# Optimization experiments

Hardware: AMD Instinct MI355X
Metric: run time of the kernel (lower is better)

## Reference

```python
import jax, jax.numpy as jnp
import numpy as np

COMMITMENT_COST = 0.25


def setup_inputs() -> dict:
    key = jax.random.key(0)
    k1, k2 = jax.random.split(key)
    inputs = jax.random.normal(k1, (8, 1024, 512), dtype=jnp.float32)
    codebook = jax.random.normal(k2, (8192, 512), dtype=jnp.float32)
    return {"inputs": inputs, "codebook": codebook}


def reference(inputs, codebook):
    B, S, D = inputs.shape
    flat = inputs.reshape(-1, D)  # [N, D]
    distances = (
        jnp.sum(flat * flat, axis=1, keepdims=True)
        + jnp.sum(codebook * codebook, axis=1)
        - 2.0 * flat @ codebook.T
    )
    encoding_indices = jnp.argmin(distances, axis=1)  # [N] int
    min_distances = jnp.min(distances, axis=1)  # [N]
    quantized = codebook[encoding_indices].reshape(inputs.shape)  # [B,S,D]
    # straight-through estimator
    quantized_st = inputs + jax.lax.stop_gradient(quantized - inputs)
    # mse losses with reduction='sum'; .detach() -> stop_gradient
    loss_vq = jnp.sum((quantized - jax.lax.stop_gradient(inputs)) ** 2)
    loss_commit = jnp.sum((inputs - jax.lax.stop_gradient(quantized)) ** 2)
    # non-EMA branch: loss = commitment_cost * loss_commit + loss_vq
    loss = loss_commit * COMMITMENT_COST + loss_vq
    return (
        quantized_st,
        loss,
        encoding_indices.reshape(B, S),
        min_distances.reshape(B, S),
        loss_commit,
    )
```

## Files before the change

### kernel.cpp

```cpp
#include <hip/hip_runtime.h>

typedef __attribute__((ext_vector_type(8)))  short short8;
typedef __attribute__((ext_vector_type(16))) float f32x16;
typedef unsigned short ushort_t;
typedef unsigned int uint32;

#define NROWS 8192
#define NCODE 8192
#define DIM   512

#define OUT_Q      0
#define OUT_LOSS   4194304
#define OUT_IDX    4194305
#define OUT_MIND   4202497
#define OUT_COMMIT 4210689

#define WS_ENORM  0
#define WS_PMIN   8192
#define WS_PIDX   73728
#define WS_LPART  147456
#define WS_BHI    150528
#define WS_BLO    2247680

__device__ inline uint32 bf16_rne(float f) {
    uint32 u = __float_as_uint(f);
    return (u + 0x7FFFu + ((u >> 16) & 1u)) >> 16;
}

__device__ inline void gload16(const ushort_t* g, ushort_t* l) {
    __builtin_amdgcn_global_load_lds(
        (const __attribute__((address_space(1))) void*)g,
        (__attribute__((address_space(3))) void*)l, 16, 0, 0);
}

__global__ __launch_bounds__(256) void conv_kernel(const float* __restrict__ x,
                                                   const float* __restrict__ cb,
                                                   ushort_t* __restrict__ ahi,
                                                   ushort_t* __restrict__ alo,
                                                   ushort_t* __restrict__ bhi,
                                                   ushort_t* __restrict__ blo,
                                                   float* __restrict__ enorm) {
    int gid  = blockIdx.x * 256 + threadIdx.x;
    bool isA = gid < 524288;
    int g    = isA ? gid : gid - 524288;
    int row  = g >> 6;
    int lane = g & 63;
    int k0   = lane * 8;
    const float* src = (isA ? x : cb) + (size_t)row * DIM + k0;
    float v[8];
    *(float4*)&v[0] = *(const float4*)src;
    *(float4*)&v[4] = *(const float4*)(src + 4);
    float s = 0.0f;
    uint32 h[8], l[8];
    #pragma unroll
    for (int i = 0; i < 8; ++i) {
        s += v[i] * v[i];
        h[i] = bf16_rne(v[i]);
        float hf = __uint_as_float(h[i] << 16);
        l[i] = bf16_rne(v[i] - hf);
    }
    int tile = (row >> 7) * 16 + (k0 >> 5);
    int rp = row & 127, kp = k0 & 31;
    int c  = (rp >> 5) * 2 + (kp >> 4);
    int L  = (rp & 31) + (((kp >> 3) & 1) << 5);
    size_t off = (size_t)tile * 4096 + c * 512 + L * 8;
    uint4 ph, pl;
    ph.x = h[0] | (h[1] << 16); ph.y = h[2] | (h[3] << 16);
    ph.z = h[4] | (h[5] << 16); ph.w = h[6] | (h[7] << 16);
    pl.x = l[0] | (l[1] << 16); pl.y = l[2] | (l[3] << 16);
    pl.z = l[4] | (l[5] << 16); pl.w = l[6] | (l[7] << 16);
    if (isA) {
        *(uint4*)(ahi + off) = ph;
        *(uint4*)(alo + off) = pl;
    } else {
        *(uint4*)(bhi + off) = ph;
        *(uint4*)(blo + off) = pl;
        #pragma unroll
        for (int o = 32; o > 0; o >>= 1) s += __shfl_down(s, o);
        if (lane == 0) enorm[row] = s;
    }
}

__global__ __launch_bounds__(256, 2) void vq_mfma_kernel(
        const ushort_t* __restrict__ ahi, const ushort_t* __restrict__ alo,
        const ushort_t* __restrict__ bhi, const ushort_t* __restrict__ blo,
        const float* __restrict__ enorm,
        float* __restrict__ pmin, int* __restrict__ pidx) {
    __shared__ __align__(16) ushort_t smem[32768];

    const int tid  = threadIdx.x;
    const int wave = tid >> 6, lane = tid & 63;
    const int l31  = lane & 31, half = lane >> 5;
    const int q  = blockIdx.x;
    const int bx = (q & 7) * 8 + (q >> 6);
    const int by = (q >> 3) & 7;
    const int wrow = (wave >> 1) * 64;
    const int wcol = (wave & 1) * 64;
    const int so = wave * 512 + lane * 8;

    f32x16 acc[2][2];
    #pragma unroll
    for (int i = 0; i < 2; ++i)
        #pragma unroll
        for (int j = 0; j < 2; ++j)
            #pragma unroll
            for (int r = 0; r < 16; ++r) acc[i][j][r] = 0.0f;

    float bestd[32];
    int   besti[32];
    #pragma unroll
    for (int i = 0; i < 32; ++i) { bestd[i] = 3.4e38f; besti[i] = 0x7FFFFFFF; }

    auto stage = [&](int n) {
        const int kb = n & 15;
        const int ctile = by * 8 + (n >> 4);
        const size_t at = (size_t)(bx * 16 + kb) * 4096;
        const size_t bt = (size_t)(ctile * 16 + kb) * 4096;
        ushort_t* S = smem + (n & 1) * 16384;
        gload16(ahi + at + so,        S + so);
        gload16(ahi + at + 2048 + so, S + 2048 + so);
        gload16(alo + at + so,        S + 4096 + so);
        gload16(alo + at + 2048 + so, S + 6144 + so);
        gload16(bhi + bt + so,        S + 8192 + so);
        gload16(bhi + bt + 2048 + so, S + 10240 + so);
        gload16(blo + bt + so,        S + 12288 + so);
        gload16(blo + bt + 2048 + so, S + 14336 + so);
    };

    stage(0);

    for (int n = 0; n < 128; ++n) {
        __syncthreads();
        if (n + 1 < 128) stage(n + 1);

        ushort_t* S = smem + (n & 1) * 16384;
        #pragma unroll
        for (int k16 = 0; k16 < 2; ++k16) {
            short8 ah[2], al[2], bh[2], bl[2];
            #pragma unroll
            for (int ti = 0; ti < 2; ++ti) {
                int ca = ((wrow >> 5) + ti) * 2 + k16;
                ah[ti] = *(const short8*)&S[ca * 512 + lane * 8];
                al[ti] = *(const short8*)&S[4096 + ca * 512 + lane * 8];
            }
            #pragma unroll
            for (int tj = 0; tj < 2; ++tj) {
                int cb_ = ((wcol >> 5) + tj) * 2 + k16;
                bh[tj] = *(const short8*)&S[8192 + cb_ * 512 + lane * 8];
                bl[tj] = *(const short8*)&S[12288 + cb_ * 512 + lane * 8];
            }
            #pragma unroll
            for (int ti = 0; ti < 2; ++ti)
                #pragma unroll
                for (int tj = 0; tj < 2; ++tj) {
                    acc[ti][tj] = __builtin_amdgcn_mfma_f32_32x32x16_bf16(
                        ah[ti], bh[tj], acc[ti][tj], 0, 0, 0);
                    acc[ti][tj] = __builtin_amdgcn_mfma_f32_32x32x16_bf16(
                        ah[ti], bl[tj], acc[ti][tj], 0, 0, 0);
                    acc[ti][tj] = __builtin_amdgcn_mfma_f32_32x32x16_bf16(
                        al[ti], bh[tj], acc[ti][tj], 0, 0, 0);
                }
        }

        if ((n & 15) == 15) {
            const int ct = n >> 4;
            const int colbase = by * 1024 + ct * 128 + wcol;
            #pragma unroll
            for (int tj = 0; tj < 2; ++tj) {
                const int ci = colbase + tj * 32 + l31;
                const float en = enorm[ci];
                #pragma unroll
                for (int ti = 0; ti < 2; ++ti)
                    #pragma unroll
                    for (int reg = 0; reg < 16; ++reg) {
                        float d = en - 2.0f * acc[ti][tj][reg];
                        int s = ti * 16 + reg;
                        if (d < bestd[s]) { bestd[s] = d; besti[s] = ci; }
                    }
            }
            #pragma unroll
            for (int i = 0; i < 2; ++i)
                #pragma unroll
                for (int j = 0; j < 2; ++j)
                    #pragma unroll
                    for (int r = 0; r < 16; ++r) acc[i][j][r] = 0.0f;
        }
    }

    float* rd = (float*)smem;
    int*   ri = (int*)smem + 8192;
    __syncthreads();
    const int slot = (wave & 1) * 32 + l31;
    #pragma unroll
    for (int ti = 0; ti < 2; ++ti)
        #pragma unroll
        for (int reg = 0; reg < 16; ++reg) {
            int row = wrow + ti * 32 + (reg & 3) + 8 * (reg >> 2) + 4 * half;
            rd[slot * 128 + row] = bestd[ti * 16 + reg];
            ri[slot * 128 + row] = besti[ti * 16 + reg];
        }
    __syncthreads();
    if (tid < 128) {
        float bd = rd[tid];
        int   bi = ri[tid];
        #pragma unroll 8
        for (int t = 1; t < 64; ++t) {
            float d = rd[t * 128 + tid];
            int  ii = ri[t * 128 + tid];
            if (d < bd || (d == bd && ii < bi)) { bd = d; bi = ii; }
        }
        pmin[(size_t)(bx * 128 + tid) * 8 + by] = bd;
        pidx[(size_t)(bx * 128 + tid) * 8 + by] = bi;
    }
}

__global__ __launch_bounds__(256) void finish_kernel(const float* __restrict__ x,
                                                     const float* __restrict__ cb,
                                                     const float* __restrict__ pmin,
                                                     const int* __restrict__ pidx,
                                                     float* __restrict__ out_idx,
                                                     float* __restrict__ qout,
                                                     float* __restrict__ out_mind,
                                                     float* __restrict__ lpart) {
    __shared__ float sred[4];
    int row  = blockIdx.x * 4 + (threadIdx.x >> 6);
    int lane = threadIdx.x & 63;

    float d = (lane < 8) ? pmin[(size_t)row * 8 + lane] : 3.4e38f;
    int  ii = (lane < 8) ? pidx[(size_t)row * 8 + lane] : 0x7FFFFFFF;
    #pragma unroll
    for (int o = 4; o > 0; o >>= 1) {
        float d2 = __shfl_down(d, o);
        int   i2 = __shfl_down(ii, o);
        if (d2 < d || (d2 == d && i2 < ii)) { d = d2; ii = i2; }
    }
    int idx = __shfl(ii, 0);
    if (lane == 0) out_idx[row] = (float)idx;

    const float4* e4 = (const float4*)(cb + (size_t)idx * DIM);
    const float4* x4 = (const float4*)(x + (size_t)row * DIM);
    float4* q4 = (float4*)(qout + (size_t)row * DIM);
    float s = 0.0f;
    #pragma unroll
    for (int u = 0; u < 2; ++u) {
        float4 e  = e4[lane + u * 64];
        float4 xv = x4[lane + u * 64];
        q4[lane + u * 64] = e;
        float dx = xv.x - e.x, dy = xv.y - e.y, dz = xv.z - e.z, dw = xv.w - e.w;
        s += dx * dx + dy * dy + dz * dz + dw * dw;
    }
    #pragma unroll
    for (int o = 32; o > 0; o >>= 1) s += __shfl_down(s, o);
    if (lane == 0) { sred[threadIdx.x >> 6] = s; out_mind[row] = s; }
    __syncthreads();
    if (threadIdx.x == 0) lpart[blockIdx.x] = sred[0] + sred[1] + sred[2] + sred[3];
}

__global__ __launch_bounds__(256) void loss_kernel(const float* __restrict__ lpart,
                                                   float* __restrict__ out_loss,
                                                   float* __restrict__ out_commit) {
    __shared__ float sm[256];
    float s = 0.0f;
    for (int i = threadIdx.x; i < 2048; i += 256) s += lpart[i];
    sm[threadIdx.x] = s;
    __syncthreads();
    #pragma unroll
    for (int o = 128; o > 0; o >>= 1) {
        if (threadIdx.x < o) sm[threadIdx.x] += sm[threadIdx.x + o];
        __syncthreads();
    }
    if (threadIdx.x == 0) {
        *out_commit = sm[0];
        *out_loss   = 1.25f * sm[0];
    }
}

extern "C" void kernel_launch(void* const* d_in, const int* in_sizes, int n_in,
                              void* d_out, int out_size, void* d_ws, size_t ws_size,
                              hipStream_t stream) {
    const float* x  = (const float*)d_in[0];
    const float* cb = (const float*)d_in[1];
    float* out = (float*)d_out;
    float* ws  = (float*)d_ws;

    ushort_t* ahi = (ushort_t*)d_out;
    ushort_t* alo = (ushort_t*)d_out + 4194304;
    ushort_t* bhi = (ushort_t*)(ws + WS_BHI);
    ushort_t* blo = (ushort_t*)(ws + WS_BLO);
    float* enorm = ws + WS_ENORM;
    float* pmin  = ws + WS_PMIN;
    int*   pidx  = (int*)(ws + WS_PIDX);
    float* lpart = ws + WS_LPART;

    conv_kernel<<<4096, 256, 0, stream>>>(x, cb, ahi, alo, bhi, blo, enorm);
    vq_mfma_kernel<<<512, 256, 0, stream>>>(ahi, alo, bhi, blo, enorm, pmin, pidx);
    finish_kernel<<<NROWS / 4, 256, 0, stream>>>(x, cb, pmin, pidx,
                                                 out + OUT_IDX, out + OUT_Q,
                                                 out + OUT_MIND, lpart);
    loss_kernel<<<1, 256, 0, stream>>>(lpart, out + OUT_LOSS, out + OUT_COMMIT);
}
```

Before: 274.8 us.

## Split A/B prefetch across k-halves with explicit waitcnt, barriers and MFMA priority

Restructures the double-buffered main loop. The A prefetch is issued before the wait and the B prefetch is moved between the LDS reads and the MFMAs, with a manual s_waitcnt vmcnt(4) and raw s_barrier replacing __syncthreads. The two k16 halves are split into separate barrier-delimited phases, MFMA issue is raised with s_setprio, and the loop is unrolled by 2. The final reduction scratch is padded to a stride of 129 to avoid LDS bank conflicts. The aim is to overlap global loads with MFMA and to cut full waitcnt stalls. The risk is that the extra barriers and the hand-tuned vmcnt accounting could add synchronization cost or become fragile.

```diff
diff --git a/kernel.cpp b/kernel.cpp
--- a/kernel.cpp
+++ b/kernel.cpp
@@ -81,12 +81,21 @@
     }
 }
 
+#define MFMA3(ti, tj) do {                                                    \
+    acc[ti][tj] = __builtin_amdgcn_mfma_f32_32x32x16_bf16(                    \
+        ah[ti], bh[tj], acc[ti][tj], 0, 0, 0);                                \
+    acc[ti][tj] = __builtin_amdgcn_mfma_f32_32x32x16_bf16(                    \
+        ah[ti], bl[tj], acc[ti][tj], 0, 0, 0);                                \
+    acc[ti][tj] = __builtin_amdgcn_mfma_f32_32x32x16_bf16(                    \
+        al[ti], bh[tj], acc[ti][tj], 0, 0, 0);                                \
+} while (0)
+
 __global__ __launch_bounds__(256, 2) void vq_mfma_kernel(
         const ushort_t* __restrict__ ahi, const ushort_t* __restrict__ alo,
         const ushort_t* __restrict__ bhi, const ushort_t* __restrict__ blo,
         const float* __restrict__ enorm,
         float* __restrict__ pmin, int* __restrict__ pidx) {
-    __shared__ __align__(16) ushort_t smem[32768];
+    __shared__ __align__(16) ushort_t smem[33024];
 
     const int tid  = threadIdx.x;
     const int wave = tid >> 6, lane = tid & 63;
@@ -111,56 +120,81 @@
     #pragma unroll
     for (int i = 0; i < 32; ++i) { bestd[i] = 3.4e38f; besti[i] = 0x7FFFFFFF; }
 
-    auto stage = [&](int n) {
-        const int kb = n & 15;
-        const int ctile = by * 8 + (n >> 4);
+    auto stageA = [&](int nn) {
+        const int kb = nn & 15;
         const size_t at = (size_t)(bx * 16 + kb) * 4096;
+        ushort_t* S2 = smem + (nn & 1) * 16384;
+        gload16(ahi + at + so,        S2 + so);
+        gload16(ahi + at + 2048 + so, S2 + 2048 + so);
+        gload16(alo + at + so,        S2 + 4096 + so);
+        gload16(alo + at + 2048 + so, S2 + 6144 + so);
+    };
+    auto stageB = [&](int nn) {
+        const int kb = nn & 15;
+        const int ctile = by * 8 + (nn >> 4);
         const size_t bt = (size_t)(ctile * 16 + kb) * 4096;
+        ushort_t* S2 = smem + (nn & 1) * 16384;
+        gload16(bhi + bt + so,        S2 + 8192 + so);
+        gload16(bhi + bt + 2048 + so, S2 + 10240 + so);
+        gload16(blo + bt + so,        S2 + 12288 + so);
+        gload16(blo + bt + 2048 + so, S2 + 14336 + so);
+    };
+
+    stageA(0); stageB(0);
+
+    #pragma unroll 2
+    for (int n = 0; n < 128; ++n) {
         ushort_t* S = smem + (n & 1) * 16384;
-        gload16(ahi + at + so,        S + so);
-        gload16(ahi + at + 2048 + so, S + 2048 + so);
-        gload16(alo + at + so,        S + 4096 + so);
-        gload16(alo + at + 2048 + so, S + 6144 + so);
-        gload16(bhi + bt + so,        S + 8192 + so);
-        gload16(bhi + bt + 2048 + so, S + 10240 + so);
-        gload16(blo + bt + so,        S + 12288 + so);
-        gload16(blo + bt + 2048 + so, S + 14336 + so);
-    };
-
-    stage(0);
-
-    for (int n = 0; n < 128; ++n) {
-        __syncthreads();
-        if (n + 1 < 128) stage(n + 1);
-
-        ushort_t* S = smem + (n & 1) * 16384;
-        #pragma unroll
-        for (int k16 = 0; k16 < 2; ++k16) {
+
+        if (n < 127) {
+            stageA(n + 1);
+            asm volatile("s_waitcnt vmcnt(4)" ::: "memory");
+        } else {
+            asm volatile("s_waitcnt vmcnt(0)" ::: "memory");
+        }
+        asm volatile("s_barrier" ::: "memory");
+        __builtin_amdgcn_sched_barrier(0);
+
+        {
             short8 ah[2], al[2], bh[2], bl[2];
             #pragma unroll
             for (int ti = 0; ti < 2; ++ti) {
-                int ca = ((wrow >> 5) + ti) * 2 + k16;
+                int ca = ((wrow >> 5) + ti) * 2;
                 ah[ti] = *(const short8*)&S[ca * 512 + lane * 8];
                 al[ti] = *(const short8*)&S[4096 + ca * 512 + lane * 8];
             }
             #pragma unroll
             for (int tj = 0; tj < 2; ++tj) {
-                int cb_ = ((wcol >> 5) + tj) * 2 + k16;
+                int cb_ = ((wcol >> 5) + tj) * 2;
                 bh[tj] = *(const short8*)&S[8192 + cb_ * 512 + lane * 8];
                 bl[tj] = *(const short8*)&S[12288 + cb_ * 512 + lane * 8];
             }
-            #pragma unroll
-            for (int ti = 0; ti < 2; ++ti)
-                #pragma unroll
-                for (int tj = 0; tj < 2; ++tj) {
-                    acc[ti][tj] = __builtin_amdgcn_mfma_f32_32x32x16_bf16(
-                        ah[ti], bh[tj], acc[ti][tj], 0, 0, 0);
-                    acc[ti][tj] = __builtin_amdgcn_mfma_f32_32x32x16_bf16(
-                        ah[ti], bl[tj], acc[ti][tj], 0, 0, 0);
-                    acc[ti][tj] = __builtin_amdgcn_mfma_f32_32x32x16_bf16(
-                        al[ti], bh[tj], acc[ti][tj], 0, 0, 0);
-                }
-        }
+            if (n < 127) stageB(n + 1);
+            __builtin_amdgcn_s_setprio(1);
+            MFMA3(0, 0); MFMA3(0, 1); MFMA3(1, 0); MFMA3(1, 1);
+            __builtin_amdgcn_s_setprio(0);
+        }
+        asm volatile("s_barrier" ::: "memory");
+
+        {
+            short8 ah[2], al[2], bh[2], bl[2];
+            #pragma unroll
+            for (int ti = 0; ti < 2; ++ti) {
+                int ca = ((wrow >> 5) + ti) * 2 + 1;
+                ah[ti] = *(const short8*)&S[ca * 512 + lane * 8];
+                al[ti] = *(const short8*)&S[4096 + ca * 512 + lane * 8];
+            }
+            #pragma unroll
+            for (int tj = 0; tj < 2; ++tj) {
+                int cb_ = ((wcol >> 5) + tj) * 2 + 1;
+                bh[tj] = *(const short8*)&S[8192 + cb_ * 512 + lane * 8];
+                bl[tj] = *(const short8*)&S[12288 + cb_ * 512 + lane * 8];
+            }
+            __builtin_amdgcn_s_setprio(1);
+            MFMA3(0, 0); MFMA3(0, 1); MFMA3(1, 0); MFMA3(1, 1);
+            __builtin_amdgcn_s_setprio(0);
+        }
+        asm volatile("s_barrier" ::: "memory");
 
         if ((n & 15) == 15) {
             const int ct = n >> 4;
@@ -188,7 +222,7 @@
     }
 
     float* rd = (float*)smem;
-    int*   ri = (int*)smem + 8192;
+    int*   ri = (int*)smem + 8256;
     __syncthreads();
     const int slot = (wave & 1) * 32 + l31;
     #pragma unroll
@@ -196,8 +230,8 @@
         #pragma unroll
         for (int reg = 0; reg < 16; ++reg) {
             int row = wrow + ti * 32 + (reg & 3) + 8 * (reg >> 2) + 4 * half;
-            rd[slot * 128 + row] = bestd[ti * 16 + reg];
-            ri[slot * 128 + row] = besti[ti * 16 + reg];
+            rd[slot * 129 + row] = bestd[ti * 16 + reg];
+            ri[slot * 129 + row] = besti[ti * 16 + reg];
         }
     __syncthreads();
     if (tid < 128) {
@@ -205,8 +239,8 @@
         int   bi = ri[tid];
         #pragma unroll 8
         for (int t = 1; t < 64; ++t) {
-            float d = rd[t * 128 + tid];
-            int  ii = ri[t * 128 + tid];
+            float d = rd[t * 129 + tid];
+            int  ii = ri[t * 129 + tid];
             if (d < bd || (d == bd && ii < bi)) { bd = d; bi = ii; }
         }
         pmin[(size_t)(bx * 128 + tid) * 8 + by] = bd;
```

Measured after the change: 280.9 us. 2.2% more time.

## Enlarge MFMA block tile to 256x256 with split A/B staging and wave-shuffle argmin

Applied to the files above, without the earlier changes.

The distance GEMM kernel moves from 256-thread blocks computing 128x128 tiles to 512-thread blocks computing 256x256 tiles, with each wave owning a 64x128 sub-tile (2x4 MFMA accumulators). This raises arithmetic intensity per byte loaded from LDS and global memory. A and B prefetches are split, with the B load issued mid-iteration, and explicit vmcnt waits, s_barrier and setprio are used around the MFMA clusters. Best indices are packed as 16-bit pairs to save registers, and the final argmin uses cross-lane shuffles instead of an LDS reduction. The larger accumulator set raises register pressure, and the grid drops to 256 blocks, which may underfill the GPU.

```diff
diff --git a/kernel.cpp b/kernel.cpp
--- a/kernel.cpp
+++ b/kernel.cpp
@@ -81,136 +81,162 @@
     }
 }
 
-__global__ __launch_bounds__(256, 2) void vq_mfma_kernel(
+__global__ __launch_bounds__(512, 2) void vq_mfma_kernel(
         const ushort_t* __restrict__ ahi, const ushort_t* __restrict__ alo,
         const ushort_t* __restrict__ bhi, const ushort_t* __restrict__ blo,
         const float* __restrict__ enorm,
         float* __restrict__ pmin, int* __restrict__ pidx) {
-    __shared__ __align__(16) ushort_t smem[32768];
+    __shared__ __align__(16) ushort_t smem[65536];
 
     const int tid  = threadIdx.x;
     const int wave = tid >> 6, lane = tid & 63;
     const int l31  = lane & 31, half = lane >> 5;
     const int q  = blockIdx.x;
-    const int bx = (q & 7) * 8 + (q >> 6);
+    const int bx = (q & 7) * 4 + (q >> 6);
     const int by = (q >> 3) & 7;
-    const int wrow = (wave >> 1) * 64;
-    const int wcol = (wave & 1) * 64;
-    const int so = wave * 512 + lane * 8;
-
-    f32x16 acc[2][2];
+    const int wr = wave >> 1;
+    const int wc = wave & 1;
+    const int wrow = wr * 64, wcol = wc * 128;
+    const int so = tid * 8;
+
+    f32x16 acc[2][4];
     #pragma unroll
     for (int i = 0; i < 2; ++i)
         #pragma unroll
-        for (int j = 0; j < 2; ++j)
+        for (int j = 0; j < 4; ++j)
             #pragma unroll
             for (int r = 0; r < 16; ++r) acc[i][j][r] = 0.0f;
 
-    float bestd[32];
-    int   besti[32];
-    #pragma unroll
-    for (int i = 0; i < 32; ++i) { bestd[i] = 3.4e38f; besti[i] = 0x7FFFFFFF; }
-
-    auto stage = [&](int n) {
-        const int kb = n & 15;
-        const int ctile = by * 8 + (n >> 4);
-        const size_t at = (size_t)(bx * 16 + kb) * 4096;
-        const size_t bt = (size_t)(ctile * 16 + kb) * 4096;
-        ushort_t* S = smem + (n & 1) * 16384;
-        gload16(ahi + at + so,        S + so);
-        gload16(ahi + at + 2048 + so, S + 2048 + so);
-        gload16(alo + at + so,        S + 4096 + so);
-        gload16(alo + at + 2048 + so, S + 6144 + so);
-        gload16(bhi + bt + so,        S + 8192 + so);
-        gload16(bhi + bt + 2048 + so, S + 10240 + so);
-        gload16(blo + bt + so,        S + 12288 + so);
-        gload16(blo + bt + 2048 + so, S + 14336 + so);
+    float  bestd[32];
+    uint32 bi2[16];
+    #pragma unroll
+    for (int i = 0; i < 32; ++i) bestd[i] = 3.4e38f;
+    #pragma unroll
+    for (int i = 0; i < 16; ++i) bi2[i] = 0u;
+
+    auto stageA = [&](int nn) {
+        const int kb = nn & 15;
+        ushort_t* S2 = smem + (nn & 1) * 32768;
+        const size_t a0 = (size_t)((2 * bx)     * 16 + kb) * 4096;
+        const size_t a1 = (size_t)((2 * bx + 1) * 16 + kb) * 4096;
+        gload16(ahi + a0 + so, S2 + so);
+        gload16(ahi + a1 + so, S2 + 4096 + so);
+        gload16(alo + a0 + so, S2 + 8192 + so);
+        gload16(alo + a1 + so, S2 + 12288 + so);
     };
-
-    stage(0);
-
-    for (int n = 0; n < 128; ++n) {
-        __syncthreads();
-        if (n + 1 < 128) stage(n + 1);
-
-        ushort_t* S = smem + (n & 1) * 16384;
+    auto stageB = [&](int nn) {
+        const int kb = nn & 15;
+        const int c0 = by * 8 + (nn >> 4) * 2;
+        ushort_t* S2 = smem + (nn & 1) * 32768;
+        const size_t b0 = (size_t)(c0       * 16 + kb) * 4096;
+        const size_t b1 = (size_t)((c0 + 1) * 16 + kb) * 4096;
+        gload16(bhi + b0 + so, S2 + 16384 + so);
+        gload16(bhi + b1 + so, S2 + 20480 + so);
+        gload16(blo + b0 + so, S2 + 24576 + so);
+        gload16(blo + b1 + so, S2 + 28672 + so);
+    };
+
+    stageA(0); stageB(0);
+
+    #pragma unroll 2
+    for (int n = 0; n < 64; ++n) {
+        ushort_t* S = smem + (n & 1) * 32768;
+
+        if (n < 63) {
+            stageA(n + 1);
+            asm volatile("s_waitcnt vmcnt(4)" ::: "memory");
+        } else {
+            asm volatile("s_waitcnt vmcnt(0)" ::: "memory");
+        }
+        asm volatile("s_barrier" ::: "memory");
+        __builtin_amdgcn_sched_barrier(0);
+
         #pragma unroll
-        for (int k16 = 0; k16 < 2; ++k16) {
-            short8 ah[2], al[2], bh[2], bl[2];
+        for (int p = 0; p < 2; ++p) {
+            short8 ah[2], al[2], bh[4], bl[4];
             #pragma unroll
             for (int ti = 0; ti < 2; ++ti) {
-                int ca = ((wrow >> 5) + ti) * 2 + k16;
-                ah[ti] = *(const short8*)&S[ca * 512 + lane * 8];
-                al[ti] = *(const short8*)&S[4096 + ca * 512 + lane * 8];
+                int c = (wr * 2 + ti) * 2 + p;
+                ah[ti] = *(const short8*)&S[c * 512 + lane * 8];
+                al[ti] = *(const short8*)&S[8192 + c * 512 + lane * 8];
             }
             #pragma unroll
-            for (int tj = 0; tj < 2; ++tj) {
-                int cb_ = ((wcol >> 5) + tj) * 2 + k16;
-                bh[tj] = *(const short8*)&S[8192 + cb_ * 512 + lane * 8];
-                bl[tj] = *(const short8*)&S[12288 + cb_ * 512 + lane * 8];
+            for (int tj = 0; tj < 4; ++tj) {
+                int c = (wc * 4 + tj) * 2 + p;
+                bh[tj] = *(const short8*)&S[16384 + c * 512 + lane * 8];
+                bl[tj] = *(const short8*)&S[24576 + c * 512 + lane * 8];
             }
+            if (p == 0 && n < 63) stageB(n + 1);
+            __builtin_amdgcn_s_setprio(1);
             #pragma unroll
             for (int ti = 0; ti < 2; ++ti)
                 #pragma unroll
-                for (int tj = 0; tj < 2; ++tj) {
+                for (int tj = 0; tj < 4; ++tj)
                     acc[ti][tj] = __builtin_amdgcn_mfma_f32_32x32x16_bf16(
                         ah[ti], bh[tj], acc[ti][tj], 0, 0, 0);
+            #pragma unroll
+            for (int ti = 0; ti < 2; ++ti)
+                #pragma unroll
+                for (int tj = 0; tj < 4; ++tj)
                     acc[ti][tj] = __builtin_amdgcn_mfma_f32_32x32x16_bf16(
                         ah[ti], bl[tj], acc[ti][tj], 0, 0, 0);
+            #pragma unroll
+            for (int ti = 0; ti < 2; ++ti)
+                #pragma unroll
+                for (int tj = 0; tj < 4; ++tj)
                     acc[ti][tj] = __builtin_amdgcn_mfma_f32_32x32x16_bf16(
                         al[ti], bh[tj], acc[ti][tj], 0, 0, 0);
-                }
-        }
+            __builtin_amdgcn_s_setprio(0);
+        }
+        asm volatile("s_barrier" ::: "memory");
 
         if ((n & 15) == 15) {
             const int ct = n >> 4;
-            const int colbase = by * 1024 + ct * 128 + wcol;
-            #pragma unroll
-            for (int tj = 0; tj < 2; ++tj) {
+            const int colbase = by * 1024 + ct * 256 + wcol;
+            #pragma unroll
+            for (int tj = 0; tj < 4; ++tj) {
                 const int ci = colbase + tj * 32 + l31;
                 const float en = enorm[ci];
                 #pragma unroll
                 for (int ti = 0; ti < 2; ++ti)
                     #pragma unroll
-                    for (int reg = 0; reg < 16; ++reg) {
-                        float d = en - 2.0f * acc[ti][tj][reg];
-                        int s = ti * 16 + reg;
-                        if (d < bestd[s]) { bestd[s] = d; besti[s] = ci; }
+                    for (int r = 0; r < 16; ++r) {
+                        float d = en - 2.0f * acc[ti][tj][r];
+                        int s = ti * 16 + r;
+                        if (d < bestd[s]) {
+                            bestd[s] = d;
+                            int sh = (s & 1) << 4;
+                            bi2[s >> 1] = (bi2[s >> 1] & (0xFFFF0000u >> sh))
+                                        | ((uint32)ci << sh);
+                        }
                     }
             }
             #pragma unroll
             for (int i = 0; i < 2; ++i)
                 #pragma unroll
-                for (int j = 0; j < 2; ++j)
+                for (int j = 0; j < 4; ++j)
                     #pragma unroll
                     for (int r = 0; r < 16; ++r) acc[i][j][r] = 0.0f;
         }
     }
 
-    float* rd = (float*)smem;
-    int*   ri = (int*)smem + 8192;
-    __syncthreads();
-    const int slot = (wave & 1) * 32 + l31;
-    #pragma unroll
-    for (int ti = 0; ti < 2; ++ti)
+    #pragma unroll
+    for (int s = 0; s < 32; ++s) {
+        float d = bestd[s];
+        int   i = (int)((bi2[s >> 1] >> ((s & 1) << 4)) & 0xFFFFu);
         #pragma unroll
-        for (int reg = 0; reg < 16; ++reg) {
+        for (int m = 16; m > 0; m >>= 1) {
+            float d2 = __shfl_xor(d, m);
+            int   i2 = __shfl_xor(i, m);
+            if (d2 < d || (d2 == d && i2 < i)) { d = d2; i = i2; }
+        }
+        if (l31 == 0) {
+            int ti = s >> 4, reg = s & 15;
             int row = wrow + ti * 32 + (reg & 3) + 8 * (reg >> 2) + 4 * half;
-            rd[slot * 128 + row] = bestd[ti * 16 + reg];
-            ri[slot * 128 + row] = besti[ti * 16 + reg];
-        }
-    __syncthreads();
-    if (tid < 128) {
-        float bd = rd[tid];
-        int   bi = ri[tid];
-        #pragma unroll 8
-        for (int t = 1; t < 64; ++t) {
-            float d = rd[t * 128 + tid];
-            int  ii = ri[t * 128 + tid];
-            if (d < bd || (d == bd && ii < bi)) { bd = d; bi = ii; }
-        }
-        pmin[(size_t)(bx * 128 + tid) * 8 + by] = bd;
-        pidx[(size_t)(bx * 128 + tid) * 8 + by] = bi;
+            size_t gr = (size_t)(bx * 256 + row);
+            pmin[gr * 8 + by] = d;
+            pidx[gr * 8 + by] = i;
+        }
     }
 }
 
@@ -293,7 +319,7 @@
     float* lpart = ws + WS_LPART;
 
     conv_kernel<<<4096, 256, 0, stream>>>(x, cb, ahi, alo, bhi, blo, enorm);
-    vq_mfma_kernel<<<512, 256, 0, stream>>>(ahi, alo, bhi, blo, enorm, pmin, pidx);
+    vq_mfma_kernel<<<256, 512, 0, stream>>>(ahi, alo, bhi, blo, enorm, pmin, pidx);
     finish_kernel<<<NROWS / 4, 256, 0, stream>>>(x, cb, pmin, pidx,
                                                  out + OUT_IDX, out + OUT_Q,
                                                  out + OUT_MIND, lpart);
```

Result: slower. 283.7 us (+3.2%).

## Widen wave tile, triple-buffer LDS and pack argmin index into float key

Applied to the files above, without the earlier changes.

Each wave's output tile grows from 64x64 to 64x128. LDS staging becomes a three-stage ring with explicit vmcnt waits. MFMA fragments are double-buffered in registers so LDS reads overlap the MFMA groups, which run under raised priority. The per-lane (distance, index) tracking is replaced by one float key whose low 13 mantissa bits hold the codebook index. This shrinks register pressure and the final reduction to shuffles plus a two-way min. In exchange, distances lose low mantissa bits, which can alter near-tie argmin results and the reported minimum distances.

```diff
diff --git a/kernel.cpp b/kernel.cpp
--- a/kernel.cpp
+++ b/kernel.cpp
@@ -81,12 +81,14 @@
     }
 }
 
+struct Frags { short8 ah[2]; short8 al[2]; short8 bh[4]; short8 bl[4]; };
+
 __global__ __launch_bounds__(256, 2) void vq_mfma_kernel(
         const ushort_t* __restrict__ ahi, const ushort_t* __restrict__ alo,
         const ushort_t* __restrict__ bhi, const ushort_t* __restrict__ blo,
         const float* __restrict__ enorm,
         float* __restrict__ pmin, int* __restrict__ pidx) {
-    __shared__ __align__(16) ushort_t smem[32768];
+    __shared__ __align__(16) ushort_t smem[36864];
 
     const int tid  = threadIdx.x;
     const int wave = tid >> 6, lane = tid & 63;
@@ -94,124 +96,149 @@
     const int q  = blockIdx.x;
     const int bx = (q & 7) * 8 + (q >> 6);
     const int by = (q >> 3) & 7;
-    const int wrow = (wave >> 1) * 64;
-    const int wcol = (wave & 1) * 64;
-    const int so = wave * 512 + lane * 8;
-
-    f32x16 acc[2][2];
+    const int wr = wave >> 1;
+    const int wc = wave & 1;
+    const int wr2 = wr * 2, wc4 = wc * 4;
+    const int l8 = lane * 8;
+
+    f32x16 acc[2][4];
     #pragma unroll
     for (int i = 0; i < 2; ++i)
         #pragma unroll
-        for (int j = 0; j < 2; ++j)
+        for (int j = 0; j < 4; ++j)
             #pragma unroll
             for (int r = 0; r < 16; ++r) acc[i][j][r] = 0.0f;
 
-    float bestd[32];
-    int   besti[32];
-    #pragma unroll
-    for (int i = 0; i < 32; ++i) { bestd[i] = 3.4e38f; besti[i] = 0x7FFFFFFF; }
-
-    auto stage = [&](int n) {
-        const int kb = n & 15;
-        const int ctile = by * 8 + (n >> 4);
-        const size_t at = (size_t)(bx * 16 + kb) * 4096;
-        const size_t bt = (size_t)(ctile * 16 + kb) * 4096;
-        ushort_t* S = smem + (n & 1) * 16384;
-        gload16(ahi + at + so,        S + so);
-        gload16(ahi + at + 2048 + so, S + 2048 + so);
-        gload16(alo + at + so,        S + 4096 + so);
-        gload16(alo + at + 2048 + so, S + 6144 + so);
-        gload16(bhi + bt + so,        S + 8192 + so);
-        gload16(bhi + bt + 2048 + so, S + 10240 + so);
-        gload16(blo + bt + so,        S + 12288 + so);
-        gload16(blo + bt + 2048 + so, S + 14336 + so);
+    float keys[32];
+    #pragma unroll
+    for (int i = 0; i < 32; ++i) keys[i] = 3.4e38f;
+
+    auto stage = [&](int nn) {
+        const int kb = nn & 31, kc = kb >> 1, k16 = kb & 1;
+        const int ct = nn >> 5;
+        ushort_t* S2 = smem + (nn % 3) * 12288;
+        const int lo = (tid >> 6) * 1024 + (k16 << 9) + (tid & 63) * 8;
+        const size_t at = ((size_t)bx * 16 + kc) << 12;
+        gload16(ahi + at + lo, S2 + tid * 8);
+        gload16(alo + at + lo, S2 + 2048 + tid * 8);
+        const int c0 = by * 8 + ct * 2;
+        const size_t bt0 = ((size_t)c0 * 16 + kc) << 12;
+        const size_t bt1 = bt0 + ((size_t)16 << 12);
+        gload16(bhi + bt0 + lo, S2 + 4096 + tid * 8);
+        gload16(bhi + bt1 + lo, S2 + 6144 + tid * 8);
+        gload16(blo + bt0 + lo, S2 + 8192 + tid * 8);
+        gload16(blo + bt1 + lo, S2 + 10240 + tid * 8);
     };
 
-    stage(0);
-
-    for (int n = 0; n < 128; ++n) {
-        __syncthreads();
-        if (n + 1 < 128) stage(n + 1);
-
-        ushort_t* S = smem + (n & 1) * 16384;
+#define RD(base) (*(const short8*)&Sr[(base) + l8])
+#define MFMA8(A, B) do {                                                      \
+    __builtin_amdgcn_s_setprio(1);                                            \
+    _Pragma("unroll")                                                         \
+    for (int ti = 0; ti < 2; ++ti)                                            \
+        _Pragma("unroll")                                                     \
+        for (int tj = 0; tj < 4; ++tj)                                        \
+            acc[ti][tj] = __builtin_amdgcn_mfma_f32_32x32x16_bf16(            \
+                (A)[ti], (B)[tj], acc[ti][tj], 0, 0, 0);                      \
+    __builtin_amdgcn_s_setprio(0);                                            \
+} while (0)
+
+#define BODY(nn, CUR, NXT) do {                                               \
+    if ((nn) + 2 < 128) {                                                     \
+        stage((nn) + 2);                                                      \
+        asm volatile("s_waitcnt vmcnt(6)" ::: "memory");                      \
+    } else {                                                                  \
+        asm volatile("s_waitcnt vmcnt(0)" ::: "memory");                      \
+    }                                                                         \
+    asm volatile("s_barrier" ::: "memory");                                   \
+    __builtin_amdgcn_sched_barrier(0);                                        \
+    const ushort_t* Sr = smem + (((nn) + 1) % 3) * 12288;                     \
+    MFMA8(CUR.ah, CUR.bh);                                            \
+    NXT.ah[0] = RD((wr2 + 0) * 512);                      \
+    NXT.ah[1] = RD((wr2 + 1) * 512);                                          \
+    NXT.bh[0] = RD(4096 + (wc4 + 0) * 512);                                   \
+    NXT.bh[1] = RD(4096 + (wc4 + 1) * 512);                                   \
+    NXT.bh[2] = RD(4096 + (wc4 + 2) * 512);                                   \
+    NXT.bh[3] = RD(4096 + (wc4 + 3) * 512);                                   \
+    MFMA8(CUR.ah, CUR.bl);                                            \
+    NXT.bl[0] = RD(8192 + (wc4 + 0) * 512);               \
+    NXT.bl[1] = RD(8192 + (wc4 + 1) * 512);                                   \
+    NXT.bl[2] = RD(8192 + (wc4 + 2) * 512);                                   \
+    NXT.bl[3] = RD(8192 + (wc4 + 3) * 512);                                   \
+    NXT.al[0] = RD(2048 + (wr2 + 0) * 512);                                   \
+    NXT.al[1] = RD(2048 + (wr2 + 1) * 512);                                   \
+    MFMA8(CUR.al, CUR.bh);                                            \
+    if (((nn) & 31) == 31) {                                                  \
+        const int ct = (nn) >> 5;                                             \
+        const int colbase = by * 1024 + ct * 256 + wc * 128;                  \
+        _Pragma("unroll")                                                     \
+        for (int tj = 0; tj < 4; ++tj) {                                      \
+            const int ci = colbase + tj * 32 + l31;                           \
+            const float en = enorm[ci];                                       \
+            _Pragma("unroll")                                                 \
+            for (int ti = 0; ti < 2; ++ti)                                    \
+                _Pragma("unroll")                                             \
+                for (int r = 0; r < 16; ++r) {                                \
+                    float d = en - 2.0f * acc[ti][tj][r];                     \
+                    float cand = __uint_as_float(                             \
+                        (__float_as_uint(d) & 0xFFFFE000u) | (uint32)ci);     \
+                    int s = ti * 16 + r;                                      \
+                    if (cand < keys[s]) keys[s] = cand;                       \
+                }                                                             \
+        }                                                                     \
+        _Pragma("unroll")                                                     \
+        for (int i = 0; i < 2; ++i)                                           \
+            _Pragma("unroll")                                                 \
+            for (int j = 0; j < 4; ++j)                                       \
+                _Pragma("unroll")                                             \
+                for (int r = 0; r < 16; ++r) acc[i][j][r] = 0.0f;             \
+    }                                                                         \
+} while (0)
+
+    Frags Fa, Fb;
+
+    stage(0); stage(1);
+    asm volatile("s_waitcnt vmcnt(6)" ::: "memory");
+    __syncthreads();
+    {
+        const ushort_t* Sr = smem;
+        Fa.ah[0] = RD((wr2 + 0) * 512);  Fa.ah[1] = RD((wr2 + 1) * 512);
+        Fa.al[0] = RD(2048 + (wr2 + 0) * 512);
+        Fa.al[1] = RD(2048 + (wr2 + 1) * 512);
         #pragma unroll
-        for (int k16 = 0; k16 < 2; ++k16) {
-            short8 ah[2], al[2], bh[2], bl[2];
-            #pragma unroll
-            for (int ti = 0; ti < 2; ++ti) {
-                int ca = ((wrow >> 5) + ti) * 2 + k16;
-                ah[ti] = *(const short8*)&S[ca * 512 + lane * 8];
-                al[ti] = *(const short8*)&S[4096 + ca * 512 + lane * 8];
-            }
-            #pragma unroll
-            for (int tj = 0; tj < 2; ++tj) {
-                int cb_ = ((wcol >> 5) + tj) * 2 + k16;
-                bh[tj] = *(const short8*)&S[8192 + cb_ * 512 + lane * 8];
-                bl[tj] = *(const short8*)&S[12288 + cb_ * 512 + lane * 8];
-            }
-            #pragma unroll
-            for (int ti = 0; ti < 2; ++ti)
-                #pragma unroll
-                for (int tj = 0; tj < 2; ++tj) {
-                    acc[ti][tj] = __builtin_amdgcn_mfma_f32_32x32x16_bf16(
-                        ah[ti], bh[tj], acc[ti][tj], 0, 0, 0);
-                    acc[ti][tj] = __builtin_amdgcn_mfma_f32_32x32x16_bf16(
-                        ah[ti], bl[tj], acc[ti][tj], 0, 0, 0);
-                    acc[ti][tj] = __builtin_amdgcn_mfma_f32_32x32x16_bf16(
-                        al[ti], bh[tj], acc[ti][tj], 0, 0, 0);
-                }
+        for (int tj = 0; tj < 4; ++tj) {
+            Fa.bh[tj] = RD(4096 + (wc4 + tj) * 512);
+            Fa.bl[tj] = RD(8192 + (wc4 + tj) * 512);
         }
-
-        if ((n & 15) == 15) {
-            const int ct = n >> 4;
-            const int colbase = by * 1024 + ct * 128 + wcol;
-            #pragma unroll
-            for (int tj = 0; tj < 2; ++tj) {
-                const int ci = colbase + tj * 32 + l31;
-                const float en = enorm[ci];
-                #pragma unroll
-                for (int ti = 0; ti < 2; ++ti)
-                    #pragma unroll
-                    for (int reg = 0; reg < 16; ++reg) {
-                        float d = en - 2.0f * acc[ti][tj][reg];
-                        int s = ti * 16 + reg;
-                        if (d < bestd[s]) { bestd[s] = d; besti[s] = ci; }
-                    }
-            }
-            #pragma unroll
-            for (int i = 0; i < 2; ++i)
-                #pragma unroll
-                for (int j = 0; j < 2; ++j)
-                    #pragma unroll
-                    for (int r = 0; r < 16; ++r) acc[i][j][r] = 0.0f;
+    }
+
+    for (int n = 0; n < 128; n += 2) {
+        BODY(n, Fa, Fb);
+        BODY(n + 1, Fb, Fa);
+    }
+
+    __syncthreads();
+    float* rd = (float*)smem;
+    #pragma unroll
+    for (int s = 0; s < 32; ++s) {
+        float k = keys[s];
+        #pragma unroll
+        for (int m = 16; m > 0; m >>= 1) k = fminf(k, __shfl_xor(k, m));
+        if (l31 == 0) {
+            int r = s & 15;
+            int row = wr * 64 + (s >> 4) * 32 + (r & 3) + 8 * (r >> 2) + 4 * half;
+            rd[wc * 128 + row] = k;
         }
     }
-
-    float* rd = (float*)smem;
-    int*   ri = (int*)smem + 8192;
-    __syncthreads();
-    const int slot = (wave & 1) * 32 + l31;
-    #pragma unroll
-    for (int ti = 0; ti < 2; ++ti)
-        #pragma unroll
-        for (int reg = 0; reg < 16; ++reg) {
-            int row = wrow + ti * 32 + (reg & 3) + 8 * (reg >> 2) + 4 * half;
-            rd[slot * 128 + row] = bestd[ti * 16 + reg];
-            ri[slot * 128 + row] = besti[ti * 16 + reg];
-        }
     __syncthreads();
     if (tid < 128) {
-        float bd = rd[tid];
-        int   bi = ri[tid];
-        #pragma unroll 8
-        for (int t = 1; t < 64; ++t) {
-            float d = rd[t * 128 + tid];
-            int  ii = ri[t * 128 + tid];
-            if (d < bd || (d == bd && ii < bi)) { bd = d; bi = ii; }
-        }
-        pmin[(size_t)(bx * 128 + tid) * 8 + by] = bd;
-        pidx[(size_t)(bx * 128 + tid) * 8 + by] = bi;
-    }
+        float k = fminf(rd[tid], rd[128 + tid]);
+        size_t gr = (size_t)bx * 128 + tid;
+        pmin[gr * 8 + by] = k;
+        pidx[gr * 8 + by] = (int)(__float_as_uint(k) & 8191u);
+    }
+#undef RD
+#undef MFMA8
+#undef BODY
 }
 
 __global__ __launch_bounds__(256) void finish_kernel(const float* __restrict__ x,
```

New measurement: 274.8 us. No clear change (-0.0%).
